# Kernel optimization log

Measured on AMD Instinct MI355X. Metric: run time of the kernel, lower is better.

The kernel has to match this reference:

```python
import jax, jax.numpy as jnp
import numpy as np
from jax import lax

D3 = 48      # manifold_dim * 3
M = 512      # mem_slots
H = 256      # slot_dim
K = 32       # topk
IN = 1024    # input_dim
ODE_HID = 128
ODE_STEPS = 2
ODE_DT = 0.5
TEMP = 1.0   # temperature buffer
LN_EPS = 1e-5


def _ln(x, g, b):
    m = jnp.mean(x, axis=-1, keepdims=True)
    v = jnp.mean(jnp.square(x - m), axis=-1, keepdims=True)
    return (x - m) * lax.rsqrt(v + LN_EPS) * g + b


def setup_inputs() -> dict:
    key = jax.random.key(0)
    ks = jax.random.split(key, 12)
    s_in = 1.0 / np.sqrt(IN)
    s_h = 1.0 / np.sqrt(H)
    s_d3 = 1.0 / np.sqrt(D3)
    s_ode = 1.0 / np.sqrt(ODE_HID)
    return {
        "x": jax.random.normal(ks[0], (16, 2048, IN), jnp.float32),
        "w1": jax.random.uniform(ks[1], (IN, D3), jnp.float32, -s_in, s_in),
        "b1": jnp.zeros((D3,), jnp.float32),
        "g1": jnp.ones((D3,), jnp.float32),
        "be1": jnp.zeros((D3,), jnp.float32),
        "wa": jax.random.uniform(ks[2], (D3, ODE_HID), jnp.float32, -s_d3, s_d3),
        "ba": jnp.zeros((ODE_HID,), jnp.float32),
        "wb": jax.random.uniform(ks[3], (ODE_HID, D3), jnp.float32, -s_ode, s_ode),
        "bb": jnp.zeros((D3,), jnp.float32),
        "mem": jax.random.normal(ks[4], (M, H), jnp.float32),
        "pos": jax.random.normal(ks[5], (M, 16, 3), jnp.float32),
        "curv": jax.random.normal(ks[6], (M, 16), jnp.float32),
        "alpha": jnp.float32(0.1),
        "wo": jax.random.uniform(ks[7], (H, IN), jnp.float32, -s_h, s_h),
        "bo": jnp.zeros((IN,), jnp.float32),
        "go": jnp.ones((IN,), jnp.float32),
        "beo": jnp.zeros((IN,), jnp.float32),
    }


def reference(x, w1, b1, g1, be1, wa, ba, wb, bb, mem, pos, curv, alpha, wo, bo, go, beo):
    # manifold projection: Linear -> LayerNorm -> GELU, viewed as (B,S,D,3)
    h = jax.nn.gelu(_ln(x @ w1 + b1, g1, be1), approximate=False)  # (B,S,48)
    # ODE evolution (2 fixed steps over the flattened manifold coords)
    for _ in range(ODE_STEPS):
        dx = jnp.tanh(h @ wa + ba) @ wb + bb
        h = h + ODE_DT * dx
    # attend: query side is detached in the original
    q = lax.stop_gradient(h)                       # (B,S,48)
    mem_pos = pos.reshape(M, -1)                   # (512,48)
    # squared pairwise L2: ||q||^2 - 2 q.m + ||m||^2
    dist = (jnp.sum(q * q, axis=-1, keepdims=True)
            - 2.0 * jnp.einsum('bsd,md->bsm', q, mem_pos)
            + jnp.sum(mem_pos * mem_pos, axis=-1))
    dist = jnp.maximum(dist, 0.0) / max(TEMP, 1e-6)
    curv_w = jnp.exp(-alpha * jnp.linalg.norm(curv, axis=-1))  # (512,)
    dist = dist * curv_w[None, None, :]
    # topk smallest distances
    neg_top, itop = lax.top_k(-dist, K)            # (B,S,K)
    w = jax.nn.softmax(neg_top, axis=-1)           # softmax(-dtop)
    slots = mem[itop]                              # (B,S,K,256) gather
    attended = jnp.einsum('bsk,bskh->bsh', w, slots)
    # output projection: Linear -> LayerNorm -> GELU
    return jax.nn.gelu(_ln(attended @ wo + bo, go, beo), approximate=False)
```

## Files before the change

kernel.cpp:

```cpp
#include <hip/hip_runtime.h>
#include <stdint.h>

typedef unsigned short u16;
typedef __attribute__((ext_vector_type(4))) short short4v;
typedef __attribute__((ext_vector_type(8))) short short8v;
typedef __attribute__((ext_vector_type(4))) float f32x4;
typedef __attribute__((address_space(1))) void gv;
typedef __attribute__((address_space(3))) void lv;

#define NTOK 32768

__device__ __forceinline__ float bf2f(u16 u){ return __uint_as_float(((uint32_t)u)<<16); }
__device__ __forceinline__ u16 f2bf(float f){
  uint32_t u = __float_as_uint(f);
  u += 0x7FFFu + ((u>>16)&1u);
  return (u16)(u>>16);
}
__device__ __forceinline__ void hilo(float v, u16& h, u16& l){
  h = f2bf(v);
  l = f2bf(v - bf2f(h));
}
__device__ __forceinline__ void tsplit(float v, u16& h, u16& l){
  uint32_t b = __float_as_uint(v);
  h = (u16)(b >> 16);
  float lf = v - __uint_as_float(b & 0xFFFF0000u);
  l = (u16)(__float_as_uint(lf) >> 16);
}
__device__ __forceinline__ void tpack8(float4 a, float4 b, short8v& hi, short8v& lo){
  float v[8] = {a.x,a.y,a.z,a.w,b.x,b.y,b.z,b.w};
  #pragma unroll
  for (int i=0;i<8;++i){ u16 h,l; tsplit(v[i],h,l); hi[i]=(short)h; lo[i]=(short)l; }
}
__device__ __forceinline__ float fexp2(float x){ float r; asm("v_exp_f32 %0, %1" : "=v"(r) : "v"(x)); return r; }
__device__ __forceinline__ float frcp(float x){ float r; asm("v_rcp_f32 %0, %1" : "=v"(r) : "v"(x)); return r; }

__device__ __forceinline__ float gelu_f(float v){ return 0.5f*v*(1.0f + erff(v*0.70710678118654752440f)); }
__device__ __forceinline__ float gelu_t(float x){
  float p = x*(2.3022141f + 0.1029435f*x*x);
  float e = fexp2(p);
  float r = frcp(e + 1.0f);
  return x*(1.0f - r);
}
__device__ __forceinline__ float tanh_f(float x){
  float e = fexp2(2.8853901f*x);
  float r = frcp(e + 1.0f);
  return 1.0f - 2.0f*r;
}

__global__ __launch_bounds__(256) void k_prep(
    const float* __restrict__ w1, const float* __restrict__ wa, const float* __restrict__ wb,
    const float* __restrict__ pos, const float* __restrict__ curv,
    const float* __restrict__ mem, const float* __restrict__ wo,
    const float* __restrict__ alpha,
    u16* __restrict__ w1s, u16* __restrict__ wah, u16* __restrict__ wbh,
    float2* __restrict__ mnw,
    u16* __restrict__ memb, u16* __restrict__ woB, u16* __restrict__ posB)
{
  int i = blockIdx.x*256 + threadIdx.x;
  if (i < 49152){ int n = i>>10, k = i&1023; u16 h,l; hilo(w1[k*48+n], h, l);
                  w1s[i] = h; w1s[49152+i] = l; return; }
  i -= 49152;
  if (i < 8192){ int u = i>>6, d = i&63; float v = (d<48) ? wa[d*128+u] : 0.f;
                 u16 h,l; hilo(v,h,l); wah[i] = h; wah[8192+i] = l; return; }
  i -= 8192;
  if (i < 6144){ int n = i>>7, u = i&127; u16 h,l; hilo(wb[u*48+n], h, l);
                 wbh[i] = h; wbh[6144+i] = l; return; }
  i -= 6144;
  if (i < 512){
    float s = 0.f;
    #pragma unroll
    for (int d=0; d<48; ++d){ float v = pos[i*48+d]; s += v*v; }
    float c2 = 0.f;
    #pragma unroll
    for (int d=0; d<16; ++d){ float v = curv[i*16+d]; c2 += v*v; }
    mnw[i] = make_float2(s, expf(-alpha[0]*sqrtf(c2)));
    return;
  }
  i -= 512;
  if (i < 131072){ memb[i] = f2bf(mem[i]); return; }
  i -= 131072;
  if (i < 262144){
    int e = i & 7, ln = (i>>3)&63, n = (i>>9)&15, cpq = (i>>13)&3, kt = i>>15;
    int col = cpq*256 + n*16 + (ln & 15);
    int k   = kt*32 + (ln >> 4)*8 + e;
    woB[i] = f2bf(wo[k*1024 + col]);
    return;
  }
  i -= 262144;
  if (i < 32768){
    int e = i & 7, ln = (i>>3)&63, n = (i>>9)&31, ks = i>>14;
    int slot = n*16 + (ln&15);
    int d = ks*32 + (ln>>4)*8 + e;
    float v = (d < 48) ? pos[slot*48 + d] : 0.f;
    u16 h,l; hilo(v,h,l);
    posB[i] = h; posB[32768+i] = l;
  }
}

__global__ __launch_bounds__(256, 2) void k_proj(
    const float* __restrict__ x, const u16* __restrict__ w1s,
    const float* __restrict__ b1, const float* __restrict__ g1, const float* __restrict__ be1,
    float* __restrict__ hout)
{
  extern __shared__ char dynp[];
  float* xsl = (float*)dynp;
  u16*   bsl = (u16*)(dynp + 49152);

  const int tid = threadIdx.x;
  const int lane = tid & 63, w = tid >> 6;
  const int l15 = lane & 15, l4 = lane >> 4;
  const int bm = blockIdx.x;
  const int arow = w*16 + l15;

  f32x4 acc[3];
  #pragma unroll
  for (int n=0; n<3; ++n) acc[n] = (f32x4){0.f,0.f,0.f,0.f};

  auto stage_x = [&](float* dst, int kt){
    #pragma unroll
    for (int j=0; j<4; ++j){
      int idx = (j*4 + w)*64 + lane;
      int row = idx >> 4, q = idx & 15;
      int chunk = q >> 1, half = q & 1;
      const float* src = x + (size_t)(bm*64 + row)*1024 + kt*64 + ((chunk ^ (row & 7))*8 + half*4);
      __builtin_amdgcn_global_load_lds((gv*)src, (lv*)(dst + (j*4 + w)*256), 16, 0, 0);
    }
  };
  auto stage_b = [&](u16* dst, int kt){
    #pragma unroll
    for (int j=0; j<3; ++j){
      int idx = (j*4 + w)*64 + lane;
      int hl = (idx >= 384) ? 1 : 0;
      int rr = idx - hl*384;
      int row = rr >> 3, ch = rr & 7;
      const u16* src = w1s + hl*49152 + (size_t)row*1024 + kt*64 + ((ch ^ (row & 7))*8);
      __builtin_amdgcn_global_load_lds((gv*)src, (lv*)(dst + (j*4 + w)*512), 16, 0, 0);
    }
  };
  auto mfma_from = [&](const float* xb, const u16* bb){
    #pragma unroll
    for (int kq=0; kq<2; ++kq){
      int chunk = kq*4 + l4;
      int phys = chunk ^ (arow & 7);
      const float* xa = xb + arow*64 + phys*8;
      float4 a0 = *(const float4*)xa;
      float4 a1 = *(const float4*)(xa + 4);
      short8v ah, al; tpack8(a0, a1, ah, al);
      #pragma unroll
      for (int n=0; n<3; ++n){
        int brow = n*16 + l15;
        int bcx = chunk ^ (brow & 7);
        short8v bh = *(const short8v*)(bb + brow*64 + bcx*8);
        short8v bl = *(const short8v*)(bb + 3072 + brow*64 + bcx*8);
        acc[n] = __builtin_amdgcn_mfma_f32_16x16x32_bf16(ah, bh, acc[n], 0, 0, 0);
        acc[n] = __builtin_amdgcn_mfma_f32_16x16x32_bf16(ah, bl, acc[n], 0, 0, 0);
        acc[n] = __builtin_amdgcn_mfma_f32_16x16x32_bf16(al, bh, acc[n], 0, 0, 0);
      }
    }
  };

  float* x0 = xsl;         float* x1 = xsl + 4096;  float* x2 = xsl + 8192;
  u16*   b0 = bsl;         u16*   b1b = bsl + 6144;

  stage_b(b0, 0);
  stage_x(x0, 0);
  stage_x(x1, 1);

  float* xc = x0; float* xn = x1; float* xn2 = x2;
  u16* bc = b0;  u16* bn = b1b;

  for (int kt = 0; kt < 15; ++kt){
    asm volatile("s_waitcnt vmcnt(4)" ::: "memory");
    __builtin_amdgcn_s_barrier();
    __builtin_amdgcn_sched_barrier(0);
    mfma_from(xc, bc);
    stage_b(bn, kt + 1);
    if (kt < 14) stage_x(xn2, kt + 2);
    { float* t = xc; xc = xn; xn = xn2; xn2 = t; }
    { u16* t = bc; bc = bn; bn = t; }
  }
  asm volatile("s_waitcnt vmcnt(0)" ::: "memory");
  __builtin_amdgcn_s_barrier();
  __builtin_amdgcn_sched_barrier(0);
  mfma_from(xc, bc);

  float b1r[3], g1r[3], e1r[3];
  #pragma unroll
  for (int n=0; n<3; ++n){ int c = n*16 + l15; b1r[n] = b1[c]; g1r[n] = g1[c]; e1r[n] = be1[c]; }
  #pragma unroll
  for (int r=0; r<4; ++r){
    float a0 = acc[0][r] + b1r[0];
    float a1 = acc[1][r] + b1r[1];
    float a2 = acc[2][r] + b1r[2];
    float s1 = a0+a1+a2;
    float s2 = a0*a0 + a1*a1 + a2*a2;
    #pragma unroll
    for (int m=1; m<16; m<<=1){ s1 += __shfl_xor(s1, m); s2 += __shfl_xor(s2, m); }
    float mean = s1 * (1.f/48.f);
    float var  = s2 * (1.f/48.f) - mean*mean;
    float rs = rsqrtf(var + 1e-5f);
    int row = bm*64 + w*16 + l4*4 + r;
    float* hb = hout + (size_t)row*48;
    hb[l15]      = gelu_f((a0-mean)*rs*g1r[0] + e1r[0]);
    hb[16+l15]   = gelu_f((a1-mean)*rs*g1r[1] + e1r[1]);
    hb[32+l15]   = gelu_f((a2-mean)*rs*g1r[2] + e1r[2]);
  }
}

__global__ __launch_bounds__(256) void k_ode(
    const float* __restrict__ hin,
    const u16* __restrict__ wah, const u16* __restrict__ wbh,
    const float* __restrict__ ba, const float* __restrict__ bb,
    float* __restrict__ hout, float* __restrict__ q2b)
{
  extern __shared__ u16 sm[];
  u16* t_hi = sm;
  u16* t_lo = sm + 8192;
  u16* h_hi = sm + 16384;
  u16* h_lo = sm + 20480;
  float* hscr = (float*)sm;

  const int tid = threadIdx.x;
  const int lane = tid & 63, w = tid >> 6;
  const int l15 = lane & 15, l4 = lane >> 4;
  const int bm = blockIdx.x;

  float4 hv4[3];
  #pragma unroll
  for (int it=0; it<3; ++it){
    int q = it*256 + tid;
    int row = q/12, c4 = q - row*12;
    hv4[it] = *(const float4*)(hin + (size_t)(bm*64 + row)*48 + c4*4);
  }
  #pragma unroll
  for (int it=0; it<3; ++it){
    int q = it*256 + tid;
    int row = q/12, c4 = q - row*12;
    *(float4*)&hscr[row*48 + c4*4] = hv4[it];
    float4 v = hv4[it];
    u16 h0,l0,h1,l1,h2,l2,h3,l3;
    tsplit(v.x,h0,l0); tsplit(v.y,h1,l1); tsplit(v.z,h2,l2); tsplit(v.w,h3,l3);
    int off = row*64 + ((c4>>1) ^ (row & 7))*8 + (c4 & 1)*4;
    short4v hv = {(short)h0,(short)h1,(short)h2,(short)h3};
    short4v lv = {(short)l0,(short)l1,(short)l2,(short)l3};
    *(short4v*)&h_hi[off] = hv;
    *(short4v*)&h_lo[off] = lv;
  }
  if (tid < 128){
    int row = tid >> 1, ch = 6 + (tid & 1);
    int off = row*64 + (ch ^ (row & 7))*8;
    uint4 z = {0u,0u,0u,0u};
    *(uint4*)&h_hi[off] = z;
    *(uint4*)&h_lo[off] = z;
  }
  __syncthreads();

  float hreg[3][4];
  #pragma unroll
  for (int n=0; n<3; ++n)
    #pragma unroll
    for (int r=0; r<4; ++r)
      hreg[n][r] = hscr[(w*16 + l4*4 + r)*48 + n*16 + l15];
  __syncthreads();

  float ba_r[8], bb_r[3];
  #pragma unroll
  for (int n=0; n<8; ++n) ba_r[n] = ba[n*16 + l15];
  #pragma unroll
  for (int n=0; n<3; ++n) bb_r[n] = bb[n*16 + l15];

  for (int s=0; s<2; ++s){
    f32x4 at[8];
    #pragma unroll
    for (int n=0; n<8; ++n) at[n] = (f32x4){0.f,0.f,0.f,0.f};
    #pragma unroll
    for (int kq=0; kq<2; ++kq){
      const int arow = w*16 + l15;
      int ac = (kq*4 + l4) ^ (arow & 7);
      short8v ah = *(const short8v*)&h_hi[arow*64 + ac*8];
      short8v al = *(const short8v*)&h_lo[arow*64 + ac*8];
      #pragma unroll
      for (int n=0; n<8; ++n){
        const u16* bp = wah + (n*16 + l15)*64 + kq*32 + l4*8;
        short8v bh = *(const short8v*)bp;
        short8v bl = *(const short8v*)(bp + 8192);
        at[n] = __builtin_amdgcn_mfma_f32_16x16x32_bf16(ah, bh, at[n], 0, 0, 0);
        at[n] = __builtin_amdgcn_mfma_f32_16x16x32_bf16(ah, bl, at[n], 0, 0, 0);
        at[n] = __builtin_amdgcn_mfma_f32_16x16x32_bf16(al, bh, at[n], 0, 0, 0);
      }
    }
    #pragma unroll
    for (int n=0; n<8; ++n)
      #pragma unroll
      for (int r=0; r<4; ++r){
        float tv = tanh_f(at[n][r] + ba_r[n]);
        u16 th, tl; tsplit(tv, th, tl);
        int row = w*16 + l4*4 + r;
        int col = n*16 + l15;
        int c = col >> 3;
        int phys = (c & 8) | ((c & 7) ^ (row & 7));
        int off = row*128 + phys*8 + (col & 7);
        t_hi[off] = th; t_lo[off] = tl;
      }
    f32x4 ad[3];
    #pragma unroll
    for (int n=0; n<3; ++n) ad[n] = (f32x4){0.f,0.f,0.f,0.f};
    #pragma unroll
    for (int kq=0; kq<4; ++kq){
      const int arow = w*16 + l15;
      int c = kq*4 + l4;
      int phys = (c & 8) | ((c & 7) ^ (arow & 7));
      short8v ah = *(const short8v*)&t_hi[arow*128 + phys*8];
      short8v al = *(const short8v*)&t_lo[arow*128 + phys*8];
      #pragma unroll
      for (int n=0; n<3; ++n){
        const u16* bp = wbh + (n*16 + l15)*128 + kq*32 + l4*8;
        short8v bh = *(const short8v*)bp;
        short8v bl = *(const short8v*)(bp + 6144);
        ad[n] = __builtin_amdgcn_mfma_f32_16x16x32_bf16(ah, bh, ad[n], 0, 0, 0);
        ad[n] = __builtin_amdgcn_mfma_f32_16x16x32_bf16(ah, bl, ad[n], 0, 0, 0);
        ad[n] = __builtin_amdgcn_mfma_f32_16x16x32_bf16(al, bh, ad[n], 0, 0, 0);
      }
    }
    #pragma unroll
    for (int n=0; n<3; ++n)
      #pragma unroll
      for (int r=0; r<4; ++r)
        hreg[n][r] += 0.5f*(ad[n][r] + bb_r[n]);
    if (s == 0){
      #pragma unroll
      for (int n=0; n<3; ++n)
        #pragma unroll
        for (int r=0; r<4; ++r){
          u16 hh, hl2; tsplit(hreg[n][r], hh, hl2);
          int row = w*16 + l4*4 + r;
          int col = n*16 + l15;
          int off = row*64 + ((col>>3) ^ (row & 7))*8 + (col & 7);
          h_hi[off] = hh; h_lo[off] = hl2;
        }
    }
  }
  #pragma unroll
  for (int r=0; r<4; ++r){
    size_t row = (size_t)(bm*64 + w*16 + l4*4 + r);
    #pragma unroll
    for (int n=0; n<3; ++n)
      hout[row*64 + n*16 + l15] = hreg[n][r];
    hout[row*64 + 48 + l15] = 0.f;
    float s2 = hreg[0][r]*hreg[0][r] + hreg[1][r]*hreg[1][r] + hreg[2][r]*hreg[2][r];
    #pragma unroll
    for (int msk=1; msk<16; msk<<=1) s2 += __shfl_xor(s2, msk);
    if (l15 == 0) q2b[row] = s2;
  }
}

__global__ __launch_bounds__(256, 4) void k_sel(
    const float* __restrict__ h, const float* __restrict__ q2b,
    const u16* __restrict__ posB, const float2* __restrict__ mnw,
    uint32_t* __restrict__ glist)
{
  __shared__ __align__(16) uint32_t tokKeys[2*4*528];

  const int tid = threadIdx.x;
  const int lane = tid & 63, w = tid >> 6;
  const int g = w >> 1, s = w & 1;
  const int l15 = lane & 15, l4 = lane >> 4;
  const int bm = blockIdx.x;

  const float* hrow = h + (size_t)(bm*32 + g*16 + l15)*64;
  float4 x0 = *(const float4*)(hrow + l4*8);
  float4 x1 = *(const float4*)(hrow + l4*8 + 4);
  float4 x2 = *(const float4*)(hrow + 32 + l4*8);
  float4 x3 = *(const float4*)(hrow + 32 + l4*8 + 4);
  short8v ah0, al0, ah1, al1;
  tpack8(x0, x1, ah0, al0);
  tpack8(x2, x3, ah1, al1);

  float4 q2v = *(const float4*)(q2b + bm*32 + g*16 + l4*4);
  float q2a[4] = {q2v.x, q2v.y, q2v.z, q2v.w};

  uint32_t kk[16][4];
  #pragma unroll
  for (int n=0; n<16; ++n){
    const u16* pb = posB + (size_t)(s*16 + n)*512 + lane*8;
    short8v bh0 = *(const short8v*)(pb);
    short8v bl0 = *(const short8v*)(pb + 32768);
    short8v bh1 = *(const short8v*)(pb + 16384);
    short8v bl1 = *(const short8v*)(pb + 49152);
    f32x4 acc = (f32x4){0.f,0.f,0.f,0.f};
    acc = __builtin_amdgcn_mfma_f32_16x16x32_bf16(ah0, bh0, acc, 0, 0, 0);
    acc = __builtin_amdgcn_mfma_f32_16x16x32_bf16(ah0, bl0, acc, 0, 0, 0);
    acc = __builtin_amdgcn_mfma_f32_16x16x32_bf16(al0, bh0, acc, 0, 0, 0);
    acc = __builtin_amdgcn_mfma_f32_16x16x32_bf16(ah1, bh1, acc, 0, 0, 0);
    acc = __builtin_amdgcn_mfma_f32_16x16x32_bf16(ah1, bl1, acc, 0, 0, 0);
    acc = __builtin_amdgcn_mfma_f32_16x16x32_bf16(al1, bh1, acc, 0, 0, 0);
    const int slot = s*256 + n*16 + l15;
    float2 mw = mnw[slot];
    #pragma unroll
    for (int r=0; r<4; ++r){
      float dd = fmaxf(q2a[r] + mw.x - 2.f*acc[r], 0.f) * mw.y;
      kk[n][r] = (__float_as_uint(dd) & 0xFFFFFE00u) | (uint32_t)slot;
    }
  }

  const int gbase = g*2112;
  const unsigned long long ltmask = (lane == 63) ? 0x7FFFFFFFFFFFFFFFull : ((1ull << lane) - 1ull);
  #pragma unroll
  for (int r=0; r<4; ++r){
    __syncthreads();
    #pragma unroll
    for (int n=0; n<16; ++n)
      tokKeys[gbase + l4*528 + s*256 + n*16 + l15] = kk[n][r];
    __syncthreads();
    uint32_t key8[2][8];
    #pragma unroll
    for (int j=0; j<2; ++j){
      *(uint4*)&key8[j][0] = *(const uint4*)&tokKeys[gbase + (s*2+j)*528 + lane*8];
      *(uint4*)&key8[j][4] = *(const uint4*)&tokKeys[gbase + (s*2+j)*528 + lane*8 + 4];
    }
    uint32_t p[2] = {0u,0u};
    for (int b=30; b>=0; --b){
      #pragma unroll
      for (int j=0; j<2; ++j){
        uint32_t c = p[j] | (1u<<b);
        int cnt = 0;
        #pragma unroll
        for (int i=0; i<8; ++i) cnt += (int)__popcll(__ballot(key8[j][i] < c));
        if (cnt <= 31) p[j] = c;
      }
    }
    #pragma unroll
    for (int j=0; j<2; ++j){
      size_t tok = (size_t)bm*32 + g*16 + (s*2+j)*4 + r;
      int base = 0;
      #pragma unroll
      for (int i=0; i<8; ++i){
        unsigned long long bal = __ballot(key8[j][i] <= p[j]);
        if (key8[j][i] <= p[j]){
          int idx = base + (int)__popcll(bal & ltmask);
          glist[tok*32 + idx] = key8[j][i];
        }
        base += (int)__popcll(bal);
      }
    }
  }
}

__global__ __launch_bounds__(256) void k_attend(
    const uint32_t* __restrict__ glist, const u16* __restrict__ memb,
    u16* __restrict__ att)
{
  const int lane = threadIdx.x & 63, w = threadIdx.x >> 6;
  const size_t tok = (size_t)blockIdx.x*4 + w;
  uint32_t lk[32];
  const uint4* lp = (const uint4*)(glist + tok*32);
  #pragma unroll
  for (int q=0; q<8; ++q) *(uint4*)&lk[q*4] = lp[q];
  uint32_t km = lk[0];
  #pragma unroll
  for (int i=1; i<32; ++i) km = min(km, lk[i]);
  const float dminf = __uint_as_float(km & 0xFFFFFE00u);

  float den = 0.f, a0=0.f, a1=0.f, a2=0.f, a3=0.f;
  #pragma unroll
  for (int i=0; i<32; ++i){
    float dk = __uint_as_float(lk[i] & 0xFFFFFE00u);
    int slot = (int)(lk[i] & 511u);
    float wg = __expf(dminf - dk);
    den += wg;
    uint2 mv = ((const uint2*)(memb + (size_t)slot*256))[lane];
    a0 += wg*bf2f((u16)(mv.x & 0xFFFFu));
    a1 += wg*bf2f((u16)(mv.x >> 16));
    a2 += wg*bf2f((u16)(mv.y & 0xFFFFu));
    a3 += wg*bf2f((u16)(mv.y >> 16));
  }
  float inv = frcp(den);
  uint32_t o0 = (uint32_t)f2bf(a0*inv) | ((uint32_t)f2bf(a1*inv) << 16);
  uint32_t o1 = (uint32_t)f2bf(a2*inv) | ((uint32_t)f2bf(a3*inv) << 16);
  ((uint2*)(att + tok*256))[lane] = make_uint2(o0, o1);
}

__global__ __launch_bounds__(1024, 4) void k_out(
    const u16* __restrict__ A, const u16* __restrict__ woB, const float* __restrict__ bo,
    const float* __restrict__ go, const float* __restrict__ beo, float* __restrict__ out)
{
  __shared__ u16 Asl[64*256];
  __shared__ float red1[16*65];
  __shared__ float red2[16*65];

  const int tid = threadIdx.x;
  const int lane = tid & 63, w = tid >> 6;
  const int l15 = lane & 15, l4 = lane >> 4;
  const int bm = blockIdx.x;

  #pragma unroll
  for (int j=0; j<2; ++j){
    int idx = j*1024 + tid;
    int row = idx >> 5, ch = idx & 31;
    int gc = (ch & 24) | ((ch & 7) ^ (row & 7));
    uint4 v = *(const uint4*)(A + (size_t)(bm*64 + row)*256 + gc*8);
    *(uint4*)&Asl[row*256 + ch*8] = v;
  }
  __syncthreads();

  f32x4 acc[4][4];
  #pragma unroll
  for (int m=0; m<4; ++m)
    #pragma unroll
    for (int n=0; n<4; ++n) acc[m][n] = (f32x4){0.f,0.f,0.f,0.f};

  #pragma unroll
  for (int kt=0; kt<8; ++kt){
    const int c = kt*4 + l4;
    short8v af[4];
    #pragma unroll
    for (int m=0; m<4; ++m){
      int arow = m*16 + l15;
      int aphys = (c & 24) | ((c & 7) ^ (arow & 7));
      af[m] = *(const short8v*)&Asl[arow*256 + aphys*8];
    }
    const u16* bbase = woB + ((size_t)kt*64 + w*4)*512 + lane*8;
    #pragma unroll
    for (int n=0; n<4; ++n){
      short8v bf = *(const short8v*)(bbase + n*512);
      #pragma unroll
      for (int m=0; m<4; ++m)
        acc[m][n] = __builtin_amdgcn_mfma_f32_16x16x32_bf16(af[m], bf, acc[m][n], 0, 0, 0);
    }
  }

  float bor[4];
  #pragma unroll
  for (int n=0; n<4; ++n) bor[n] = bo[w*64 + n*16 + l15];

  float s1[4][4], s2[4][4];
  #pragma unroll
  for (int m=0; m<4; ++m)
    #pragma unroll
    for (int r=0; r<4; ++r){ s1[m][r] = 0.f; s2[m][r] = 0.f; }
  #pragma unroll
  for (int m=0; m<4; ++m)
    #pragma unroll
    for (int n=0; n<4; ++n)
      #pragma unroll
      for (int r=0; r<4; ++r){
        float v = acc[m][n][r] + bor[n];
        acc[m][n][r] = v;
        s1[m][r] += v; s2[m][r] += v*v;
      }
  #pragma unroll
  for (int m=0; m<4; ++m)
    #pragma unroll
    for (int r=0; r<4; ++r){
      #pragma unroll
      for (int msk=1; msk<16; msk<<=1){
        s1[m][r] += __shfl_xor(s1[m][r], msk);
        s2[m][r] += __shfl_xor(s2[m][r], msk);
      }
    }
  if (l15 == 0){
    #pragma unroll
    for (int m=0; m<4; ++m)
      #pragma unroll
      for (int r=0; r<4; ++r){
        int t = m*16 + l4*4 + r;
        red1[w*65 + t] = s1[m][r];
        red2[w*65 + t] = s2[m][r];
      }
  }
  __syncthreads();

  float mean[4][4], rs[4][4];
  #pragma unroll
  for (int m=0; m<4; ++m)
    #pragma unroll
    for (int r=0; r<4; ++r){
      int t = m*16 + l4*4 + r;
      float a1 = red1[l15*65 + t];
      float a2 = red2[l15*65 + t];
      #pragma unroll
      for (int msk=1; msk<16; msk<<=1){
        a1 += __shfl_xor(a1, msk);
        a2 += __shfl_xor(a2, msk);
      }
      float mu = a1 * (1.f/1024.f);
      float var = a2 * (1.f/1024.f) - mu*mu;
      mean[m][r] = mu;
      rs[m][r] = rsqrtf(var + 1e-5f);
    }

  float gor[4], eor[4];
  #pragma unroll
  for (int n=0; n<4; ++n){
    int col = w*64 + n*16 + l15;
    gor[n] = go[col]; eor[n] = beo[col];
  }
  #pragma unroll
  for (int m=0; m<4; ++m)
    #pragma unroll
    for (int r=0; r<4; ++r){
      size_t row = (size_t)bm*64 + m*16 + l4*4 + r;
      float* op = out + row*1024 + w*64 + l15;
      float mu = mean[m][r], rv = rs[m][r];
      #pragma unroll
      for (int n=0; n<4; ++n){
        op[n*16] = gelu_t((acc[m][n][r] - mu)*rv*gor[n] + eor[n]);
      }
    }
}

extern "C" void kernel_launch(void* const* d_in, const int* in_sizes, int n_in,
                              void* d_out, int out_size, void* d_ws, size_t ws_size,
                              hipStream_t stream) {
  const float* x    = (const float*)d_in[0];
  const float* w1   = (const float*)d_in[1];
  const float* b1   = (const float*)d_in[2];
  const float* g1   = (const float*)d_in[3];
  const float* be1  = (const float*)d_in[4];
  const float* wa   = (const float*)d_in[5];
  const float* ba   = (const float*)d_in[6];
  const float* wb   = (const float*)d_in[7];
  const float* bb   = (const float*)d_in[8];
  const float* mem  = (const float*)d_in[9];
  const float* pos  = (const float*)d_in[10];
  const float* curv = (const float*)d_in[11];
  const float* alpha= (const float*)d_in[12];
  const float* wo   = (const float*)d_in[13];
  const float* bo   = (const float*)d_in[14];
  const float* go   = (const float*)d_in[15];
  const float* beo  = (const float*)d_in[16];
  float* out = (float*)d_out;

  char* ws = (char*)d_ws;
  size_t o = 0;
  auto take = [&](size_t b) -> char* { char* p = ws + o; o += (b + 255) & ~(size_t)255; return p; };
  char*  regA   = take(67108864);
  float* hbuf48 = (float*)regA;
  float* hbuf64 = (float*)(regA + 6291456);
  float* q2b    = (float*)(regA + 6291456 + 8388608);
  u16*   att    = (u16*)take(16777216);
  u16*   w1s    = (u16*)take(196608);
  u16*   wah    = (u16*)take(32768);
  u16*   wbh    = (u16*)take(24576);
  float2* mnw   = (float2*)take(4096);
  u16*   memb   = (u16*)take(262144);
  u16*   woB    = (u16*)take(524288);
  u16*   posB   = (u16*)take(131072);
  uint32_t* glist = (uint32_t*)take(4194304);

  hipFuncSetAttribute((const void*)k_ode, hipFuncAttributeMaxDynamicSharedMemorySize, 49152);
  hipFuncSetAttribute((const void*)k_proj, hipFuncAttributeMaxDynamicSharedMemorySize, 73728);

  k_prep<<<1914, 256, 0, stream>>>(w1, wa, wb, pos, curv, mem, wo, alpha,
                                   w1s, wah, wbh, mnw, memb, woB, posB);
  k_proj<<<512, 256, 73728, stream>>>(x, w1s, b1, g1, be1, hbuf48);
  k_ode<<<512, 256, 49152, stream>>>(hbuf48, wah, wbh, ba, bb, hbuf64, q2b);
  k_sel<<<1024, 256, 0, stream>>>(hbuf64, q2b, posB, mnw, glist);
  k_attend<<<8192, 256, 0, stream>>>(glist, memb, att);
  k_out<<<512, 1024, 0, stream>>>(att, woB, bo, go, beo, out);
  (void)in_sizes; (void)n_in; (void)out_size; (void)ws_size;
}
```

Before: 255.3 us.

## Fuse projection and ODE kernels, restructure output LayerNorm reduction

```diff
diff --git a/kernel.cpp b/kernel.cpp
--- a/kernel.cpp
+++ b/kernel.cpp
@@ -97,14 +97,20 @@
   }
 }
 
-__global__ __launch_bounds__(256, 2) void k_proj(
+__global__ __launch_bounds__(256, 2) void k_proj_ode(
     const float* __restrict__ x, const u16* __restrict__ w1s,
     const float* __restrict__ b1, const float* __restrict__ g1, const float* __restrict__ be1,
-    float* __restrict__ hout)
+    const u16* __restrict__ wah, const u16* __restrict__ wbh,
+    const float* __restrict__ ba, const float* __restrict__ bb,
+    float* __restrict__ hout, float* __restrict__ q2b)
 {
   extern __shared__ char dynp[];
   float* xsl = (float*)dynp;
   u16*   bsl = (u16*)(dynp + 49152);
+  u16* t_hi = (u16*)dynp;
+  u16* t_lo = (u16*)(dynp + 16384);
+  u16* h_hi = (u16*)(dynp + 32768);
+  u16* h_lo = (u16*)(dynp + 40960);
 
   const int tid = threadIdx.x;
   const int lane = tid & 63, w = tid >> 6;
@@ -184,84 +190,47 @@
   __builtin_amdgcn_sched_barrier(0);
   mfma_from(xc, bc);
 
-  float b1r[3], g1r[3], e1r[3];
-  #pragma unroll
-  for (int n=0; n<3; ++n){ int c = n*16 + l15; b1r[n] = b1[c]; g1r[n] = g1[c]; e1r[n] = be1[c]; }
-  #pragma unroll
-  for (int r=0; r<4; ++r){
-    float a0 = acc[0][r] + b1r[0];
-    float a1 = acc[1][r] + b1r[1];
-    float a2 = acc[2][r] + b1r[2];
-    float s1 = a0+a1+a2;
-    float s2 = a0*a0 + a1*a1 + a2*a2;
-    #pragma unroll
-    for (int m=1; m<16; m<<=1){ s1 += __shfl_xor(s1, m); s2 += __shfl_xor(s2, m); }
-    float mean = s1 * (1.f/48.f);
-    float var  = s2 * (1.f/48.f) - mean*mean;
-    float rs = rsqrtf(var + 1e-5f);
-    int row = bm*64 + w*16 + l4*4 + r;
-    float* hb = hout + (size_t)row*48;
-    hb[l15]      = gelu_f((a0-mean)*rs*g1r[0] + e1r[0]);
-    hb[16+l15]   = gelu_f((a1-mean)*rs*g1r[1] + e1r[1]);
-    hb[32+l15]   = gelu_f((a2-mean)*rs*g1r[2] + e1r[2]);
-  }
-}
-
-__global__ __launch_bounds__(256) void k_ode(
-    const float* __restrict__ hin,
-    const u16* __restrict__ wah, const u16* __restrict__ wbh,
-    const float* __restrict__ ba, const float* __restrict__ bb,
-    float* __restrict__ hout, float* __restrict__ q2b)
-{
-  extern __shared__ u16 sm[];
-  u16* t_hi = sm;
-  u16* t_lo = sm + 8192;
-  u16* h_hi = sm + 16384;
-  u16* h_lo = sm + 20480;
-  float* hscr = (float*)sm;
-
-  const int tid = threadIdx.x;
-  const int lane = tid & 63, w = tid >> 6;
-  const int l15 = lane & 15, l4 = lane >> 4;
-  const int bm = blockIdx.x;
-
-  float4 hv4[3];
-  #pragma unroll
-  for (int it=0; it<3; ++it){
-    int q = it*256 + tid;
-    int row = q/12, c4 = q - row*12;
-    hv4[it] = *(const float4*)(hin + (size_t)(bm*64 + row)*48 + c4*4);
-  }
-  #pragma unroll
-  for (int it=0; it<3; ++it){
-    int q = it*256 + tid;
-    int row = q/12, c4 = q - row*12;
-    *(float4*)&hscr[row*48 + c4*4] = hv4[it];
-    float4 v = hv4[it];
-    u16 h0,l0,h1,l1,h2,l2,h3,l3;
-    tsplit(v.x,h0,l0); tsplit(v.y,h1,l1); tsplit(v.z,h2,l2); tsplit(v.w,h3,l3);
-    int off = row*64 + ((c4>>1) ^ (row & 7))*8 + (c4 & 1)*4;
-    short4v hv = {(short)h0,(short)h1,(short)h2,(short)h3};
-    short4v lv = {(short)l0,(short)l1,(short)l2,(short)l3};
-    *(short4v*)&h_hi[off] = hv;
-    *(short4v*)&h_lo[off] = lv;
-  }
-  if (tid < 128){
-    int row = tid >> 1, ch = 6 + (tid & 1);
+  float hreg[3][4];
+  {
+    float b1r[3], g1r[3], e1r[3];
+    #pragma unroll
+    for (int n=0; n<3; ++n){ int c = n*16 + l15; b1r[n] = b1[c]; g1r[n] = g1[c]; e1r[n] = be1[c]; }
+    #pragma unroll
+    for (int r=0; r<4; ++r){
+      float a0 = acc[0][r] + b1r[0];
+      float a1 = acc[1][r] + b1r[1];
+      float a2 = acc[2][r] + b1r[2];
+      float s1 = a0+a1+a2;
+      float s2 = a0*a0 + a1*a1 + a2*a2;
+      #pragma unroll
+      for (int m=1; m<16; m<<=1){ s1 += __shfl_xor(s1, m); s2 += __shfl_xor(s2, m); }
+      float mean = s1 * (1.f/48.f);
+      float var  = s2 * (1.f/48.f) - mean*mean;
+      float rs = rsqrtf(var + 1e-5f);
+      hreg[0][r] = gelu_f((a0-mean)*rs*g1r[0] + e1r[0]);
+      hreg[1][r] = gelu_f((a1-mean)*rs*g1r[1] + e1r[1]);
+      hreg[2][r] = gelu_f((a2-mean)*rs*g1r[2] + e1r[2]);
+    }
+  }
+
+  if (l4 < 2){
+    int row = w*16 + l15;
+    int ch = 6 + l4;
     int off = row*64 + (ch ^ (row & 7))*8;
     uint4 z = {0u,0u,0u,0u};
     *(uint4*)&h_hi[off] = z;
     *(uint4*)&h_lo[off] = z;
   }
-  __syncthreads();
-
-  float hreg[3][4];
   #pragma unroll
   for (int n=0; n<3; ++n)
     #pragma unroll
-    for (int r=0; r<4; ++r)
-      hreg[n][r] = hscr[(w*16 + l4*4 + r)*48 + n*16 + l15];
-  __syncthreads();
+    for (int r=0; r<4; ++r){
+      u16 hh, hl2; tsplit(hreg[n][r], hh, hl2);
+      int row = w*16 + l4*4 + r;
+      int col = n*16 + l15;
+      int off = row*64 + ((col>>3) ^ (row & 7))*8 + (col & 7);
+      h_hi[off] = hh; h_lo[off] = hl2;
+    }
 
   float ba_r[8], bb_r[3];
   #pragma unroll
@@ -275,7 +244,6 @@
     for (int n=0; n<8; ++n) at[n] = (f32x4){0.f,0.f,0.f,0.f};
     #pragma unroll
     for (int kq=0; kq<2; ++kq){
-      const int arow = w*16 + l15;
       int ac = (kq*4 + l4) ^ (arow & 7);
       short8v ah = *(const short8v*)&h_hi[arow*64 + ac*8];
       short8v al = *(const short8v*)&h_lo[arow*64 + ac*8];
@@ -307,7 +275,6 @@
     for (int n=0; n<3; ++n) ad[n] = (f32x4){0.f,0.f,0.f,0.f};
     #pragma unroll
     for (int kq=0; kq<4; ++kq){
-      const int arow = w*16 + l15;
       int c = kq*4 + l4;
       int phys = (c & 8) | ((c & 7) ^ (arow & 7));
       short8v ah = *(const short8v*)&t_hi[arow*128 + phys*8];
@@ -485,8 +452,9 @@
     const float* __restrict__ go, const float* __restrict__ beo, float* __restrict__ out)
 {
   __shared__ u16 Asl[64*256];
-  __shared__ float red1[16*65];
-  __shared__ float red2[16*65];
+  __shared__ float redS1[64][65];
+  __shared__ float redS2[64][65];
+  __shared__ float finM[64], finR[64];
 
   const int tid = threadIdx.x;
   const int lane = tid & 63, w = tid >> 6;
@@ -552,42 +520,49 @@
   for (int m=0; m<4; ++m)
     #pragma unroll
     for (int r=0; r<4; ++r){
-      #pragma unroll
-      for (int msk=1; msk<16; msk<<=1){
-        s1[m][r] += __shfl_xor(s1[m][r], msk);
-        s2[m][r] += __shfl_xor(s2[m][r], msk);
-      }
-    }
-  if (l15 == 0){
+      s1[m][r] += __shfl_xor(s1[m][r], 1);
+      s2[m][r] += __shfl_xor(s2[m][r], 1);
+      s1[m][r] += __shfl_xor(s1[m][r], 2);
+      s2[m][r] += __shfl_xor(s2[m][r], 2);
+    }
+  if ((l15 & 3) == 0){
+    int q = l15 >> 2;
     #pragma unroll
     for (int m=0; m<4; ++m)
       #pragma unroll
       for (int r=0; r<4; ++r){
-        int t = m*16 + l4*4 + r;
-        red1[w*65 + t] = s1[m][r];
-        red2[w*65 + t] = s2[m][r];
+        int row = m*16 + l4*4 + r;
+        redS1[row][w*4 + q] = s1[m][r];
+        redS2[row][w*4 + q] = s2[m][r];
       }
   }
   __syncthreads();
 
-  float mean[4][4], rs[4][4];
-  #pragma unroll
-  for (int m=0; m<4; ++m)
-    #pragma unroll
-    for (int r=0; r<4; ++r){
-      int t = m*16 + l4*4 + r;
-      float a1 = red1[l15*65 + t];
-      float a2 = red2[l15*65 + t];
-      #pragma unroll
-      for (int msk=1; msk<16; msk<<=1){
-        a1 += __shfl_xor(a1, msk);
-        a2 += __shfl_xor(a2, msk);
-      }
+  {
+    int row = w*4 + (lane >> 4);
+    int p0 = lane & 15;
+    float a1 = redS1[row][p0] + redS1[row][p0+16] + redS1[row][p0+32] + redS1[row][p0+48];
+    float a2 = redS2[row][p0] + redS2[row][p0+16] + redS2[row][p0+32] + redS2[row][p0+48];
+    #pragma unroll
+    for (int msk=1; msk<16; msk<<=1){
+      a1 += __shfl_xor(a1, msk);
+      a2 += __shfl_xor(a2, msk);
+    }
+    if (p0 == 0){
       float mu = a1 * (1.f/1024.f);
       float var = a2 * (1.f/1024.f) - mu*mu;
-      mean[m][r] = mu;
-      rs[m][r] = rsqrtf(var + 1e-5f);
-    }
+      finM[row] = mu;
+      finR[row] = rsqrtf(var + 1e-5f);
+    }
+  }
+  __syncthreads();
+
+  float4 muv[4], rsv[4];
+  #pragma unroll
+  for (int m=0; m<4; ++m){
+    muv[m] = *(const float4*)&finM[m*16 + l4*4];
+    rsv[m] = *(const float4*)&finR[m*16 + l4*4];
+  }
 
   float gor[4], eor[4];
   #pragma unroll
@@ -601,7 +576,8 @@
     for (int r=0; r<4; ++r){
       size_t row = (size_t)bm*64 + m*16 + l4*4 + r;
       float* op = out + row*1024 + w*64 + l15;
-      float mu = mean[m][r], rv = rs[m][r];
+      float mu = ((const float*)&muv[m])[r];
+      float rv = ((const float*)&rsv[m])[r];
       #pragma unroll
       for (int n=0; n<4; ++n){
         op[n*16] = gelu_t((acc[m][n][r] - mu)*rv*gor[n] + eor[n]);
@@ -635,7 +611,6 @@
   size_t o = 0;
   auto take = [&](size_t b) -> char* { char* p = ws + o; o += (b + 255) & ~(size_t)255; return p; };
   char*  regA   = take(67108864);
-  float* hbuf48 = (float*)regA;
   float* hbuf64 = (float*)(regA + 6291456);
   float* q2b    = (float*)(regA + 6291456 + 8388608);
   u16*   att    = (u16*)take(16777216);
@@ -648,13 +623,12 @@
   u16*   posB   = (u16*)take(131072);
   uint32_t* glist = (uint32_t*)take(4194304);
 
-  hipFuncSetAttribute((const void*)k_ode, hipFuncAttributeMaxDynamicSharedMemorySize, 49152);
-  hipFuncSetAttribute((const void*)k_proj, hipFuncAttributeMaxDynamicSharedMemorySize, 73728);
+  hipFuncSetAttribute((const void*)k_proj_ode, hipFuncAttributeMaxDynamicSharedMemorySize, 73728);
 
   k_prep<<<1914, 256, 0, stream>>>(w1, wa, wb, pos, curv, mem, wo, alpha,
                                    w1s, wah, wbh, mnw, memb, woB, posB);
-  k_proj<<<512, 256, 73728, stream>>>(x, w1s, b1, g1, be1, hbuf48);
-  k_ode<<<512, 256, 49152, stream>>>(hbuf48, wah, wbh, ba, bb, hbuf64, q2b);
+  k_proj_ode<<<512, 256, 73728, stream>>>(x, w1s, b1, g1, be1, wah, wbh, ba, bb,
+                                          hbuf64, q2b);
   k_sel<<<1024, 256, 0, stream>>>(hbuf64, q2b, posB, mnw, glist);
   k_attend<<<8192, 256, 0, stream>>>(glist, memb, att);
   k_out<<<512, 1024, 0, stream>>>(att, woB, bo, go, beo, out);
```

Result: faster. 244.9 us (-4.0%).
